# Kernel optimization log

Hardware: AMD Instinct MI355X
Metric: run time of the kernel (lower is better)

Reference implementation:

```python
import jax, jax.numpy as jnp
import numpy as np

NUM_HEADS = 16
WINDOW = 64


def setup_inputs() -> dict:
    key = jax.random.key(0)
    ks = jax.random.split(key, 6)
    b, l, d = 2, 2048, 1024
    s = 1.0 / np.sqrt(d)
    return {
        "x": jax.random.normal(ks[0], (b, l, d), dtype=jnp.float32),
        "Wq": jax.random.normal(ks[1], (d, d), dtype=jnp.float32) * s,
        "Wk": jax.random.normal(ks[2], (d, d), dtype=jnp.float32) * s,
        "Wv": jax.random.normal(ks[3], (d, d), dtype=jnp.float32) * s,
        "Wo": jax.random.normal(ks[4], (d, d), dtype=jnp.float32) * s,
        "bo": jax.random.normal(ks[5], (d,), dtype=jnp.float32) * 0.01,
    }


def reference(x, Wq, Wk, Wv, Wo, bo):
    b, l, d = x.shape
    h, w = NUM_HEADS, WINDOW
    dh = d // h
    p = w // 2
    # Projections. Padding is zeros and proj_k/proj_v have no bias, so
    # padding-then-projecting equals projecting-then-zero-padding.
    q = (x @ Wq.T).reshape(b, l, h, dh)                     # (b,l,h,dh)
    xp = jnp.pad(x, ((0, 0), (p, p), (0, 0)))               # (b,l+2p,d)
    k = (xp @ Wk.T).reshape(b, l + 2 * p, h, dh)
    v = (xp @ Wv.T).reshape(b, l + 2 * p, h, dh)
    # Sliding windows: query i attends to padded positions i .. i+w-1
    win_idx = jnp.arange(l)[:, None] + jnp.arange(w)[None, :]  # (l,w)
    kw = k[:, win_idx]                                       # (b,l,w,h,dh)
    vw = v[:, win_idx]                                       # (b,l,w,h,dh)
    scale = 1.0 / np.float32(np.sqrt(dh))
    scores = jnp.einsum('blhd,blwhd->blhw', q, kw) * scale   # (b,l,h,w)
    attn = jax.nn.softmax(scores, axis=-1)
    out = jnp.einsum('blhw,blwhd->blhd', attn, vw).reshape(b, l, d)
    return out @ Wo.T + bo
```

## Files before the change

### kernel.cpp

```cpp
#include <hip/hip_runtime.h>
#include <hip/hip_bf16.h>
#include <cstdint>

typedef __bf16 bf16;
typedef __bf16 bf16x4 __attribute__((ext_vector_type(4)));
typedef __bf16 bf16x8 __attribute__((ext_vector_type(8)));
typedef float floatx4 __attribute__((ext_vector_type(4)));

typedef __attribute__((address_space(1))) void as1_void;
typedef __attribute__((address_space(3))) void as3_void;

__device__ __forceinline__ void gld16(const void* g, void* l) {
#if __has_builtin(__builtin_amdgcn_global_load_lds)
  __builtin_amdgcn_global_load_lds((as1_void*)(uintptr_t)g, (as3_void*)l, 16, 0, 0);
#else
  *(uint4*)l = *(const uint4*)g;
#endif
}

__global__ __launch_bounds__(256) void convert_kernel(
    const float* __restrict__ x, const float* __restrict__ wq,
    const float* __restrict__ wk, const float* __restrict__ wv,
    const float* __restrict__ wo, bf16* __restrict__ xbf,
    bf16* __restrict__ wqkv, bf16* __restrict__ wob) {
  int i = blockIdx.x * 256 + threadIdx.x;
  const float* src;
  bf16* dst;
  int off;
  if (i < 1048576) {
    src = x; dst = xbf; off = i;
  } else if (i < 1310720) {
    src = wq; dst = wqkv; off = i - 1048576;
  } else if (i < 1572864) {
    src = wk; dst = wqkv + 1048576; off = i - 1310720;
  } else if (i < 1835008) {
    src = wv; dst = wqkv + 2097152; off = i - 1572864;
  } else {
    src = wo; dst = wob; off = i - 1835008;
  }
  float4 v = ((const float4*)src)[off];
  bf16x4 o;
  o[0] = (bf16)v.x; o[1] = (bf16)v.y; o[2] = (bf16)v.z; o[3] = (bf16)v.w;
  ((bf16x4*)dst)[off] = o;
}

template <int MODE, int BN>
__global__ __launch_bounds__(256) void gemm_nt(const bf16* __restrict__ A,
                                               const bf16* __restrict__ Bm,
                                               bf16* __restrict__ Cb,
                                               float* __restrict__ Cf,
                                               const float* __restrict__ bias,
                                               int M, int N, int K) {
  constexpr int WN = BN / 2;
  constexpr int NI = WN / 16;
  __shared__ __attribute__((aligned(16))) bf16 As[128 * 32];
  __shared__ __attribute__((aligned(16))) bf16 Bs[BN * 32];
  const int tid = threadIdx.x;
  const int lane = tid & 63;
  const int wave = tid >> 6;
  const int quad = lane >> 4;
  const int n0 = lane & 15;
  const int wm = wave >> 1;
  const int wn = wave & 1;
  const int bN = blockIdx.x, bM = blockIdx.y;
  const bf16* Ab = A + (size_t)bM * 128 * K;
  const bf16* Bb = Bm + (size_t)bN * BN * K;
  const int c0 = tid, c1 = tid + 256;
  floatx4 acc[4][NI] = {};
  for (int k0 = 0; k0 < K; k0 += 32) {
    gld16(Ab + (size_t)(c0 >> 2) * K + k0 + (c0 & 3) * 8, &As[c0 * 8]);
    gld16(Ab + (size_t)(c1 >> 2) * K + k0 + (c1 & 3) * 8, &As[c1 * 8]);
#pragma unroll
    for (int cc = 0; cc < BN * 4; cc += 256) {
      const int c = cc + tid;
      gld16(Bb + (size_t)(c >> 2) * K + k0 + (c & 3) * 8, &Bs[c * 8]);
    }
    __syncthreads();
    bf16x8 af[4], bfr[NI];
#pragma unroll
    for (int mi = 0; mi < 4; ++mi)
      af[mi] = *(const bf16x8*)&As[(wm * 64 + mi * 16 + n0) * 32 + quad * 8];
#pragma unroll
    for (int ni = 0; ni < NI; ++ni)
      bfr[ni] = *(const bf16x8*)&Bs[(wn * WN + ni * 16 + n0) * 32 + quad * 8];
#pragma unroll
    for (int mi = 0; mi < 4; ++mi)
#pragma unroll
      for (int ni = 0; ni < NI; ++ni)
        acc[mi][ni] = __builtin_amdgcn_mfma_f32_16x16x32_bf16(
            af[mi], bfr[ni], acc[mi][ni], 0, 0, 0);
    __syncthreads();
  }
  const int rowBase = bM * 128 + wm * 64;
  const int colBase = bN * BN + wn * WN;
#pragma unroll
  for (int ni = 0; ni < NI; ++ni) {
    const int col = colBase + ni * 16 + n0;
    float badd = 0.f;
    if (MODE == 1) badd = bias[col];
#pragma unroll
    for (int mi = 0; mi < 4; ++mi)
#pragma unroll
      for (int r = 0; r < 4; ++r) {
        const int row = rowBase + mi * 16 + quad * 4 + r;
        if (MODE == 0)
          Cb[(size_t)row * N + col] = (bf16)acc[mi][ni][r];
        else
          Cf[(size_t)row * N + col] = acc[mi][ni][r] + badd;
      }
  }
}

__global__ __launch_bounds__(256) void attn_kernel(const bf16* __restrict__ qkv,
                                                   bf16* __restrict__ aout) {
  __shared__ __attribute__((aligned(16))) bf16 Ks[128 * 72];
  __shared__ __attribute__((aligned(16))) bf16 VsPs[128 * 72];
  __shared__ __attribute__((aligned(16))) bf16 Vt[64 * 136];
  const int bid = blockIdx.x;
  const int b = bid >> 9;
  const int h = (bid >> 5) & 15;
  const int i0 = (bid & 31) * 64;
  const int tid = threadIdx.x;
  const int wave = tid >> 6, lane = tid & 63;
  const int quad = lane >> 4, n0 = lane & 15;
  bf16* Vs = VsPs;

#pragma unroll
  for (int it = 0; it < 4; ++it) {
    const int idx = it * 256 + tid;
    const int r = idx >> 3, c = idx & 7;
    const int j = i0 - 32 + r;
    uint4 kv_ = make_uint4(0u, 0u, 0u, 0u);
    uint4 vv = make_uint4(0u, 0u, 0u, 0u);
    if (j >= 0 && j < 2048) {
      const bf16* base = qkv + (size_t)(b * 2048 + j) * 3072 + 1024 + h * 64 + c * 8;
      kv_ = *(const uint4*)base;
      vv = *(const uint4*)(base + 1024);
    }
    *(uint4*)&Ks[r * 72 + c * 8] = kv_;
    *(uint4*)&Vs[r * 72 + c * 8] = vv;
  }
  __syncthreads();

#pragma unroll
  for (int it = 0; it < 4; ++it) {
    const int idx = it * 256 + tid;
    const int t = idx & 127, c = idx >> 7;
    bf16x8 v = *(const bf16x8*)&Vs[t * 72 + c * 8];
#pragma unroll
    for (int jj = 0; jj < 8; ++jj) Vt[(c * 8 + jj) * 136 + t] = v[jj];
  }
  __syncthreads();

  bf16x8 aq[2];
#pragma unroll
  for (int ks = 0; ks < 2; ++ks)
    aq[ks] = *(const bf16x8*)(qkv +
        (size_t)(b * 2048 + i0 + wave * 16 + n0) * 3072 + h * 64 + ks * 32 + quad * 8);

  floatx4 accS[8] = {};
#pragma unroll
  for (int nt = 0; nt < 8; ++nt)
#pragma unroll
    for (int ks = 0; ks < 2; ++ks) {
      bf16x8 bk = *(const bf16x8*)&Ks[(nt * 16 + n0) * 72 + ks * 32 + quad * 8];
      accS[nt] = __builtin_amdgcn_mfma_f32_16x16x32_bf16(aq[ks], bk, accS[nt], 0, 0, 0);
    }

  float mrow[4] = {-1e30f, -1e30f, -1e30f, -1e30f};
#pragma unroll
  for (int nt = 0; nt < 8; ++nt)
#pragma unroll
    for (int r = 0; r < 4; ++r) {
      const int q64 = wave * 16 + quad * 4 + r;
      const int t = nt * 16 + n0;
      float s = accS[nt][r] * 0.125f;
      if (t < q64 || t >= q64 + 64) s = -1e30f;
      accS[nt][r] = s;
      mrow[r] = fmaxf(mrow[r], s);
    }
#pragma unroll
  for (int off = 1; off < 16; off <<= 1)
#pragma unroll
    for (int r = 0; r < 4; ++r)
      mrow[r] = fmaxf(mrow[r], __shfl_xor(mrow[r], off));
  float lrow[4] = {0.f, 0.f, 0.f, 0.f};
#pragma unroll
  for (int nt = 0; nt < 8; ++nt)
#pragma unroll
    for (int r = 0; r < 4; ++r) {
      const float e = __expf(accS[nt][r] - mrow[r]);
      accS[nt][r] = e;
      lrow[r] += e;
    }
#pragma unroll
  for (int off = 1; off < 16; off <<= 1)
#pragma unroll
    for (int r = 0; r < 4; ++r) lrow[r] += __shfl_xor(lrow[r], off);

  bf16* Pw = &VsPs[wave * 16 * 136];
#pragma unroll
  for (int r = 0; r < 4; ++r) {
    const float inv = 1.f / lrow[r];
#pragma unroll
    for (int nt = 0; nt < 8; ++nt)
      Pw[(quad * 4 + r) * 136 + nt * 16 + n0] = (bf16)(accS[nt][r] * inv);
  }

  floatx4 accO[4] = {};
#pragma unroll
  for (int kt = 0; kt < 4; ++kt) {
    bf16x8 ap = *(const bf16x8*)&Pw[n0 * 136 + kt * 32 + quad * 8];
#pragma unroll
    for (int dt = 0; dt < 4; ++dt) {
      bf16x8 bv = *(const bf16x8*)&Vt[(dt * 16 + n0) * 136 + kt * 32 + quad * 8];
      accO[dt] = __builtin_amdgcn_mfma_f32_16x16x32_bf16(ap, bv, accO[dt], 0, 0, 0);
    }
  }
#pragma unroll
  for (int dt = 0; dt < 4; ++dt)
#pragma unroll
    for (int r = 0; r < 4; ++r) {
      const int q64 = wave * 16 + quad * 4 + r;
      aout[(size_t)(b * 2048 + i0 + q64) * 1024 + h * 64 + dt * 16 + n0] =
          (bf16)accO[dt][r];
    }
}

extern "C" void kernel_launch(void* const* d_in, const int* in_sizes, int n_in,
                              void* d_out, int out_size, void* d_ws, size_t ws_size,
                              hipStream_t stream) {
  const float* x = (const float*)d_in[0];
  const float* wq = (const float*)d_in[1];
  const float* wk = (const float*)d_in[2];
  const float* wv = (const float*)d_in[3];
  const float* wo = (const float*)d_in[4];
  const float* bo = (const float*)d_in[5];
  char* ws = (char*)d_ws;
  bf16* xbf = (bf16*)(ws);
  bf16* wqkv = (bf16*)(ws + (8u << 20));
  bf16* wob = (bf16*)(ws + (14u << 20));
  bf16* qkv = (bf16*)(ws + (16u << 20));
  bf16* aout = xbf;

  convert_kernel<<<8192, 256, 0, stream>>>(x, wq, wk, wv, wo, xbf, wqkv, wob);
  gemm_nt<0, 128><<<dim3(24, 32), 256, 0, stream>>>(xbf, wqkv, qkv, nullptr,
                                                    nullptr, 4096, 3072, 1024);
  attn_kernel<<<1024, 256, 0, stream>>>(qkv, aout);
  gemm_nt<1, 64><<<dim3(16, 32), 256, 0, stream>>>(aout, wob, nullptr,
                                                   (float*)d_out, bo, 4096, 1024,
                                                   1024);
}
```

Baseline: 158.5 us.

## Replace QKV projection GEMM with 256x256 double-buffered swizzled pipelined kernel

Adds a new 512-thread GEMM kernel with 256x256 output tiles, a 128 KB LDS double buffer with XOR-swizzled layout, and an 8-phase schedule interleaving global-to-LDS staging with MFMA compute, plus raised wave priority during MFMA. It replaces the 128x128 QKV projection GEMM to raise data reuse per tile and overlap loads with compute. The larger tile gives only 192 blocks on a GPU with many CUs, which may leave some compute units idle, and the hand-placed waitcnt and barrier schedule is fragile.

After: 154.3 us. -2.7%, faster.

```diff
diff --git a/kernel.cpp b/kernel.cpp
--- a/kernel.cpp
+++ b/kernel.cpp
@@ -111,6 +111,132 @@
   }
 }
 
+#define BAR asm volatile("s_barrier" ::: "memory")
+#define LGKM0                                         \
+  do {                                                \
+    asm volatile("s_waitcnt lgkmcnt(0)" ::: "memory");\
+    __builtin_amdgcn_sched_barrier(0);                \
+  } while (0)
+
+#define STAGE(buf, op, h, t)                                                   \
+  do {                                                                         \
+    const char* g_ = ((op) ? Bb : Ab) + (size_t)(h) * 128 * Kb +               \
+                     (size_t)(t) * 128 + rowOff;                               \
+    char* l_ = lds + (buf) * 65536 + (op) * 32768 + (h) * 16384 + tid * 16;    \
+    gld16(g_, l_);                                                             \
+    gld16(g_ + 64 * Kb, l_ + 8192);                                            \
+  } while (0)
+
+#define LDA(buf, mh)                                                           \
+  do {                                                                         \
+    _Pragma("unroll") for (int q = 0; q < 4; ++q)                              \
+      _Pragma("unroll") for (int ks = 0; ks < 2; ++ks)                         \
+        aR[q][ks] = *(const bf16x8*)(lds + (buf) * 65536 + wm * 16384 +        \
+            ((mh) * 64 + q * 16 + n0) * 128 + ((ks * 64 + quad * 16) ^ swz));  \
+  } while (0)
+
+#define LDB(buf, g)                                                            \
+  do {                                                                         \
+    _Pragma("unroll") for (int j = 0; j < 2; ++j)                              \
+      _Pragma("unroll") for (int ks = 0; ks < 2; ++ks) {                       \
+        const int row_ = wn * 64 + ((g) * 2 + j) * 16 + n0;                    \
+        bR[g][j][ks] = *(const bf16x8*)(lds + (buf) * 65536 + 32768 +          \
+            (row_ >> 7) * 16384 + (row_ & 127) * 128 +                         \
+            ((ks * 64 + quad * 16) ^ swz));                                    \
+      }                                                                        \
+  } while (0)
+
+#define MM(mh, nh)                                                             \
+  do {                                                                         \
+    __builtin_amdgcn_s_setprio(1);                                             \
+    _Pragma("unroll") for (int q = 0; q < 4; ++q)                              \
+      _Pragma("unroll") for (int j = 0; j < 2; ++j)                            \
+        _Pragma("unroll") for (int ks = 0; ks < 2; ++ks)                       \
+          acc[(mh) * 4 + q][(nh) * 2 + j] =                                    \
+              __builtin_amdgcn_mfma_f32_16x16x32_bf16(                         \
+                  aR[q][ks], bR[nh][j][ks],                                    \
+                  acc[(mh) * 4 + q][(nh) * 2 + j], 0, 0, 0);                   \
+    __builtin_amdgcn_s_setprio(0);                                             \
+  } while (0)
+
+__global__ __launch_bounds__(512, 2) void gemm256_nt(
+    const bf16* __restrict__ A, const bf16* __restrict__ Bm,
+    bf16* __restrict__ C, int M, int N, int K) {
+  __shared__ __attribute__((aligned(16))) char lds[131072];
+  const int tid = threadIdx.x;
+  const int lane = tid & 63, wave = tid >> 6;
+  const int quad = lane >> 4, n0 = lane & 15;
+  const int wm = wave >> 2, wn = wave & 3;
+  const int swz = (n0 & 7) << 4;
+  const size_t Kb = (size_t)K * 2;
+  const char* Ab = (const char*)(A + (size_t)blockIdx.y * 256 * K);
+  const char* Bb = (const char*)(Bm + (size_t)blockIdx.x * 256 * K);
+  const int srow = tid >> 3;
+  const size_t rowOff = (size_t)srow * Kb + (size_t)(16 * ((tid & 7) ^ (srow & 7)));
+
+  floatx4 acc[8][4] = {};
+  bf16x8 aR[4][2];
+  bf16x8 bR[2][2][2];
+
+  const int NT = K >> 6;
+  const int NI = K >> 7;
+
+  STAGE(0, 0, 0, 0); STAGE(0, 0, 1, 0); STAGE(0, 1, 0, 0); STAGE(0, 1, 1, 0);
+  STAGE(1, 1, 0, 1); STAGE(1, 0, 0, 1);
+  asm volatile("s_waitcnt vmcnt(4)" ::: "memory");
+  BAR;
+
+  for (int i = 0; i < NI; ++i) {
+    const int T = 2 * i;
+    const bool s2 = (T + 2 < NT), s3 = (T + 3 < NT);
+    LDB(0, 0); LDA(0, 0);
+    STAGE(1, 0, 1, T + 1);
+    BAR; LGKM0; MM(0, 0); BAR;
+    LDB(0, 1);
+    STAGE(1, 1, 1, T + 1);
+    BAR; LGKM0; MM(0, 1); BAR;
+    LDA(0, 1);
+    if (s2) STAGE(0, 1, 0, T + 2);
+    BAR; LGKM0; MM(1, 0); BAR;
+    if (s2) STAGE(0, 1, 1, T + 2);
+    BAR; MM(1, 1);
+    if (i + 1 < NI) { asm volatile("s_waitcnt vmcnt(4)" ::: "memory"); }
+    else           { asm volatile("s_waitcnt vmcnt(0)" ::: "memory"); }
+    BAR;
+    LDB(1, 0); LDA(1, 0);
+    if (s2) STAGE(0, 0, 0, T + 2);
+    BAR; LGKM0; MM(0, 0); BAR;
+    LDB(1, 1);
+    if (s2) STAGE(0, 0, 1, T + 2);
+    BAR; LGKM0; MM(0, 1); BAR;
+    LDA(1, 1);
+    if (s3) STAGE(1, 1, 0, T + 3);
+    BAR; LGKM0; MM(1, 0); BAR;
+    if (s3) STAGE(1, 0, 0, T + 3);
+    BAR; MM(1, 1);
+    asm volatile("s_waitcnt vmcnt(4)" ::: "memory");
+    BAR;
+  }
+
+  const int rowBase = blockIdx.y * 256 + wm * 128 + quad * 4;
+  const int colBase = blockIdx.x * 256 + wn * 64 + n0;
+#pragma unroll
+  for (int mi = 0; mi < 8; ++mi)
+#pragma unroll
+    for (int ni = 0; ni < 4; ++ni)
+#pragma unroll
+      for (int r = 0; r < 4; ++r)
+        C[(size_t)(rowBase + mi * 16 + r) * N + colBase + ni * 16] =
+            (bf16)acc[mi][ni][r];
+}
+
+#undef BAR
+#undef LGKM0
+#undef STAGE
+#undef LDA
+#undef LDB
+#undef MM
+
 __global__ __launch_bounds__(256) void attn_kernel(const bf16* __restrict__ qkv,
                                                    bf16* __restrict__ aout) {
   __shared__ __attribute__((aligned(16))) bf16 Ks[128 * 72];
@@ -244,8 +370,7 @@
   bf16* aout = xbf;
 
   convert_kernel<<<8192, 256, 0, stream>>>(x, wq, wk, wv, wo, xbf, wqkv, wob);
-  gemm_nt<0, 128><<<dim3(24, 32), 256, 0, stream>>>(xbf, wqkv, qkv, nullptr,
-                                                    nullptr, 4096, 3072, 1024);
+  gemm256_nt<<<dim3(12, 16), 512, 0, stream>>>(xbf, wqkv, qkv, 4096, 3072, 1024);
   attn_kernel<<<1024, 256, 0, stream>>>(qkv, aout);
   gemm_nt<1, 64><<<dim3(16, 32), 256, 0, stream>>>(aout, wob, nullptr,
                                                    (float*)d_out, bo, 4096, 1024,
```
